# Kernel tuning notes

Hardware: AMD Instinct MI355X
Metric: run time of the kernel (lower is better)

The kernel has to match this reference:

```python
import jax, jax.numpy as jnp
import numpy as np

D = 1024

def setup_inputs() -> dict:
    key = jax.random.key(0)
    ks = jax.random.split(key, 7)
    x = jax.random.normal(ks[0], (8, 2048, D), dtype=jnp.float32)
    s = 1.0 / np.sqrt(D)
    Wq = jax.random.normal(ks[1], (D, D), dtype=jnp.float32) * s
    Wk = jax.random.normal(ks[2], (D, D), dtype=jnp.float32) * s
    Wv = jax.random.normal(ks[3], (D, D), dtype=jnp.float32) * s
    bq = jax.random.normal(ks[4], (D,), dtype=jnp.float32) * 0.01
    bk = jax.random.normal(ks[5], (D,), dtype=jnp.float32) * 0.01
    bv = jax.random.normal(ks[6], (D,), dtype=jnp.float32) * 0.01
    return {"x": x, "Wq": Wq, "bq": bq, "Wk": Wk, "bk": bk, "Wv": Wv, "bv": bv}

def reference(x, Wq, bq, Wk, bk, Wv, bv):
    # x: [b, s, d]; Linear stored as [d_in, d_out]
    Q = jnp.einsum('bsd,de->bse', x, Wq) + bq
    K = jnp.einsum('bsd,de->bse', x, Wk) + bk
    V = jnp.einsum('bsd,de->bse', x, Wv) + bv
    scale = 1.0 / jnp.sqrt(jnp.float32(x.shape[-1]))
    scores = jnp.einsum('bqd,bkd->bqk', Q, K) * scale  # [b, s, s]
    attn = jax.nn.softmax(scores, axis=-1)
    return jnp.einsum('bqk,bkd->bqd', attn, V)
```

## Files before the change

kernel.cpp:

```cpp
#include <hip/hip_runtime.h>
#include <hip/hip_bf16.h>
#include <stdint.h>

typedef __bf16 bf16x8 __attribute__((ext_vector_type(8)));
typedef float  f32x4  __attribute__((ext_vector_type(4)));

#define AS1 __attribute__((address_space(1)))
#define AS3 __attribute__((address_space(3)))

__device__ __forceinline__ void gemm_mainloop_256(
    const __hip_bfloat16* __restrict__ A,
    const __hip_bfloat16* __restrict__ B,
    int K, int m0, int n0, f32x4 acc[8][4])
{
    __shared__ __hip_bfloat16 As[2][256 * 64];
    __shared__ __hip_bfloat16 Bs[2][256 * 64];

    const int tid  = threadIdx.x;
    const int lane = tid & 63;
    const int w    = tid >> 6;
    const int wr   = w >> 2;
    const int wc   = w & 3;
    const int fr   = lane & 15;
    const int fq   = lane >> 4;
    const int lr   = lane >> 3;
    const int swz  = ((lane & 7) ^ lr) * 8;

    #pragma unroll
    for (int rt = 0; rt < 8; ++rt)
        #pragma unroll
        for (int ct = 0; ct < 4; ++ct)
            acc[rt][ct] = (f32x4){0.f, 0.f, 0.f, 0.f};

    const __hip_bfloat16* gA = A + (long)(m0 + w * 8 + lr) * K + swz;
    const __hip_bfloat16* gB = B + (long)(n0 + w * 8 + lr) * K + swz;
    const int ldsBase = (w * 8) * 64;
    const int NT = K >> 6;

#define STAGE(T, BUF)                                                        \
    {                                                                        \
        const long koff = (long)(T) * 64;                                    \
        _Pragma("unroll")                                                    \
        for (int i = 0; i < 4; ++i) {                                        \
            __builtin_amdgcn_global_load_lds(                                \
                (AS1 void*)(void*)(gA + (long)i * 64 * K + koff),            \
                (AS3 void*)(&As[BUF][ldsBase + i * 64 * 64]), 16, 0, 0);     \
            __builtin_amdgcn_global_load_lds(                                \
                (AS1 void*)(void*)(gB + (long)i * 64 * K + koff),            \
                (AS3 void*)(&Bs[BUF][ldsBase + i * 64 * 64]), 16, 0, 0);     \
        }                                                                    \
    }

    STAGE(0, 0);
    STAGE(1, 1);
    asm volatile("s_waitcnt vmcnt(8)" ::: "memory");
    __builtin_amdgcn_sched_barrier(0);
    __builtin_amdgcn_s_barrier();
    __builtin_amdgcn_sched_barrier(0);

    int cur = 0;
    for (int t = 0; t < NT; ++t) {
        #pragma unroll
        for (int ks = 0; ks < 2; ++ks) {
            const int colOff = ((ks * 4 + fq) ^ (fr & 7)) * 8;
            bf16x8 af[8], bfv[4];
            #pragma unroll
            for (int rt = 0; rt < 8; ++rt)
                af[rt] = *(const bf16x8*)&As[cur][(wr * 128 + rt * 16 + fr) * 64 + colOff];
            #pragma unroll
            for (int ct = 0; ct < 4; ++ct)
                bfv[ct] = *(const bf16x8*)&Bs[cur][(wc * 64 + ct * 16 + fr) * 64 + colOff];
            __builtin_amdgcn_s_setprio(1);
            #pragma unroll
            for (int rt = 0; rt < 8; ++rt)
                #pragma unroll
                for (int ct = 0; ct < 4; ++ct)
                    acc[rt][ct] = __builtin_amdgcn_mfma_f32_16x16x32_bf16(
                        af[rt], bfv[ct], acc[rt][ct], 0, 0, 0);
            __builtin_amdgcn_s_setprio(0);
        }
        if (t == NT - 1) break;
        __builtin_amdgcn_s_barrier();
        __builtin_amdgcn_sched_barrier(0);
        if (t + 2 < NT) {
            STAGE(t + 2, cur);
            asm volatile("s_waitcnt vmcnt(8)" ::: "memory");
        } else {
            asm volatile("s_waitcnt vmcnt(0)" ::: "memory");
        }
        __builtin_amdgcn_sched_barrier(0);
        __builtin_amdgcn_s_barrier();
        __builtin_amdgcn_sched_barrier(0);
        cur ^= 1;
    }
#undef STAGE
}

__global__ __launch_bounds__(256) void k_castx(const float* __restrict__ x,
                                               __hip_bfloat16* __restrict__ xb)
{
    int i = blockIdx.x * 256 + threadIdx.x;
    float4 f = ((const float4*)x)[i];
    union { uint2 u; __hip_bfloat16 h[4]; } o;
    o.h[0] = __float2bfloat16(f.x);
    o.h[1] = __float2bfloat16(f.y);
    o.h[2] = __float2bfloat16(f.z);
    o.h[3] = __float2bfloat16(f.w);
    ((uint2*)xb)[i] = o.u;
}

__global__ __launch_bounds__(256) void k_wt(const float* __restrict__ Wq,
                                            const float* __restrict__ Wk,
                                            const float* __restrict__ Wv,
                                            __hip_bfloat16* __restrict__ Wt)
{
    __shared__ float t[32][33];
    const float* W = (blockIdx.z == 0) ? Wq : (blockIdx.z == 1 ? Wk : Wv);
    const int d0 = blockIdx.y * 32, e0 = blockIdx.x * 32;
    #pragma unroll
    for (int j = 0; j < 4; ++j)
        t[threadIdx.y + j * 8][threadIdx.x] =
            W[(long)(d0 + threadIdx.y + j * 8) * 1024 + e0 + threadIdx.x];
    __syncthreads();
    __hip_bfloat16* dst = Wt + (long)blockIdx.z * 1024 * 1024;
    #pragma unroll
    for (int j = 0; j < 4; ++j)
        dst[(long)(e0 + threadIdx.y + j * 8) * 1024 + d0 + threadIdx.x] =
            __float2bfloat16(t[threadIdx.x][threadIdx.y + j * 8]);
}

__global__ __launch_bounds__(256) void k_zero(float* __restrict__ p)
{
    p[blockIdx.x * 256 + threadIdx.x] = 0.f;
}

__global__ __launch_bounds__(512, 2) void k_qkv(
    const __hip_bfloat16* __restrict__ xb, const __hip_bfloat16* __restrict__ Wt,
    __hip_bfloat16* __restrict__ Qb, __hip_bfloat16* __restrict__ Kb,
    __hip_bfloat16* __restrict__ Vt,
    const float* __restrict__ bq, const float* __restrict__ bk,
    const float* __restrict__ bv)
{
    f32x4 acc[8][4];
    const int n0 = blockIdx.x * 256;
    const int m0 = blockIdx.y * 256;
    gemm_mainloop_256(xb, Wt, 1024, m0, n0, acc);

    const int lane = threadIdx.x & 63, w = threadIdx.x >> 6;
    const int wr = w >> 2, wc = w & 3, fr = lane & 15, fq = lane >> 4;
    const int mat  = n0 >> 10;
    const int rowB = m0 + wr * 128;

    if (mat < 2) {
        __hip_bfloat16* out = (mat == 0) ? Qb : Kb;
        const float* bias   = (mat == 0) ? bq : bk;
        #pragma unroll
        for (int ct = 0; ct < 4; ++ct) {
            const int e = (n0 & 1023) + wc * 64 + ct * 16 + fr;
            const float bval = bias[e];
            #pragma unroll
            for (int rt = 0; rt < 8; ++rt) {
                const int r0 = rowB + rt * 16 + fq * 4;
                #pragma unroll
                for (int r = 0; r < 4; ++r)
                    out[(long)(r0 + r) * 1024 + e] =
                        __float2bfloat16(acc[rt][ct][r] + bval);
            }
        }
    } else {
        #pragma unroll
        for (int ct = 0; ct < 4; ++ct) {
            const int e = (n0 & 1023) + wc * 64 + ct * 16 + fr;
            const float bval = bv[e];
            #pragma unroll
            for (int rt = 0; rt < 8; ++rt) {
                const int r0 = rowB + rt * 16 + fq * 4;
                const int bz = r0 >> 11, s0 = r0 & 2047;
                union { ushort4 v; __hip_bfloat16 h[4]; } pk;
                #pragma unroll
                for (int r = 0; r < 4; ++r)
                    pk.h[r] = __float2bfloat16(acc[rt][ct][r] + bval);
                *(ushort4*)&Vt[(long)bz * 2097152 + (long)e * 2048 + s0] = pk.v;
            }
        }
    }
}

__global__ __launch_bounds__(512, 2) void k_scores(
    const __hip_bfloat16* __restrict__ Qb, const __hip_bfloat16* __restrict__ Kb,
    __hip_bfloat16* __restrict__ Sb, float* __restrict__ rs)
{
    f32x4 acc[8][4];
    const int z  = blockIdx.z;
    const int n0 = blockIdx.x * 256;
    const int m0 = blockIdx.y * 256;
    gemm_mainloop_256(Qb + (long)z * 2048 * 1024,
                      Kb + (long)z * 2048 * 1024, 1024, m0, n0, acc);

    __hip_bfloat16* out = Sb + (long)z * 2048 * 2048;
    float* rsz = rs + z * 2048;
    const int lane = threadIdx.x & 63, w = threadIdx.x >> 6;
    const int wr = w >> 2, wc = w & 3, fr = lane & 15, fq = lane >> 4;

    #pragma unroll
    for (int rt = 0; rt < 8; ++rt) {
        const int r0 = m0 + wr * 128 + rt * 16 + fq * 4;
        float psum[4] = {0.f, 0.f, 0.f, 0.f};
        #pragma unroll
        for (int ct = 0; ct < 4; ++ct) {
            const int col = n0 + wc * 64 + ct * 16 + fr;
            #pragma unroll
            for (int r = 0; r < 4; ++r) {
                const float p = __expf(acc[rt][ct][r] * 0.03125f);
                psum[r] += p;
                out[(long)(r0 + r) * 2048 + col] = __float2bfloat16(p);
            }
        }
        #pragma unroll
        for (int r = 0; r < 4; ++r) {
            float v = psum[r];
            v += __shfl_xor(v, 1, 16);
            v += __shfl_xor(v, 2, 16);
            v += __shfl_xor(v, 4, 16);
            v += __shfl_xor(v, 8, 16);
            if (fr == 0) atomicAdd(&rsz[r0 + r], v);
        }
    }
}

__global__ __launch_bounds__(512, 2) void k_pv(
    const __hip_bfloat16* __restrict__ Pb, const __hip_bfloat16* __restrict__ Vt,
    const float* __restrict__ rs, float* __restrict__ O)
{
    f32x4 acc[8][4];
    const int z  = blockIdx.z;
    const int n0 = blockIdx.x * 256;
    const int m0 = blockIdx.y * 256;
    gemm_mainloop_256(Pb + (long)z * 2048 * 2048,
                      Vt + (long)z * 1024 * 2048, 2048, m0, n0, acc);

    float* out = O + (long)z * 2048 * 1024;
    const float* rsz = rs + z * 2048;
    const int lane = threadIdx.x & 63, w = threadIdx.x >> 6;
    const int wr = w >> 2, wc = w & 3, fr = lane & 15, fq = lane >> 4;

    #pragma unroll
    for (int rt = 0; rt < 8; ++rt) {
        const int r0 = m0 + wr * 128 + rt * 16 + fq * 4;
        const float4 rv = *(const float4*)&rsz[r0];
        f32x4 inv;
        inv[0] = 1.f / rv.x; inv[1] = 1.f / rv.y;
        inv[2] = 1.f / rv.z; inv[3] = 1.f / rv.w;
        #pragma unroll
        for (int ct = 0; ct < 4; ++ct) {
            const int col = n0 + wc * 64 + ct * 16 + fr;
            #pragma unroll
            for (int r = 0; r < 4; ++r)
                out[(long)(r0 + r) * 1024 + col] = acc[rt][ct][r] * inv[r];
        }
    }
}

extern "C" void kernel_launch(void* const* d_in, const int* in_sizes, int n_in,
                              void* d_out, int out_size, void* d_ws, size_t ws_size,
                              hipStream_t stream)
{
    const float* x  = (const float*)d_in[0];
    const float* Wq = (const float*)d_in[1];
    const float* bq = (const float*)d_in[2];
    const float* Wk = (const float*)d_in[3];
    const float* bk = (const float*)d_in[4];
    const float* Wv = (const float*)d_in[5];
    const float* bv = (const float*)d_in[6];
    float* out = (float*)d_out;

    uint8_t* ws = (uint8_t*)d_ws;
    __hip_bfloat16* xb = (__hip_bfloat16*)(ws + 0);
    __hip_bfloat16* Wt = (__hip_bfloat16*)(ws + 33554432);
    __hip_bfloat16* Qb = (__hip_bfloat16*)(ws + 39845888);
    __hip_bfloat16* Kb = (__hip_bfloat16*)(ws + 73400320);
    __hip_bfloat16* Vt = (__hip_bfloat16*)(ws + 106954752);
    __hip_bfloat16* Sb = (__hip_bfloat16*)(ws + 140509184);
    float* rs = (float*)(ws + 33554432);

    k_castx<<<16384, 256, 0, stream>>>(x, xb);
    k_wt<<<dim3(32, 32, 3), dim3(32, 8), 0, stream>>>(Wq, Wk, Wv, Wt);
    k_qkv<<<dim3(12, 64), 512, 0, stream>>>(xb, Wt, Qb, Kb, Vt, bq, bk, bv);
    k_zero<<<64, 256, 0, stream>>>(rs);
    k_scores<<<dim3(8, 8, 8), 512, 0, stream>>>(Qb, Kb, Sb, rs);
    k_pv<<<dim3(4, 8, 8), 512, 0, stream>>>(Sb, Vt, rs, out);
}
```

Measured before the change: 404.4 us.

## Shrink GEMM tiles to 128x128 single-buffered with XCD-aware block swizzle

Replaces the 256x256 double-buffered GEMM mainloop with a 128x128 tile, 4-wave, single-buffered loop that uses plain __syncthreads, and raises occupancy targets to 3 blocks per CU. Adds an XCD block-index swizzle so that neighbouring tiles land on the same chiplet for L2 reuse. Grids grow fourfold. The change drops the async prefetch overlap and the setprio scheduling hints, and smaller tiles lower arithmetic intensity per LDS load.

```diff
diff --git a/kernel.cpp b/kernel.cpp
--- a/kernel.cpp
+++ b/kernel.cpp
@@ -8,92 +8,71 @@
 #define AS1 __attribute__((address_space(1)))
 #define AS3 __attribute__((address_space(3)))
 
-__device__ __forceinline__ void gemm_mainloop_256(
+__device__ __forceinline__ void gemm_mainloop_128(
     const __hip_bfloat16* __restrict__ A,
     const __hip_bfloat16* __restrict__ B,
-    int K, int m0, int n0, f32x4 acc[8][4])
-{
-    __shared__ __hip_bfloat16 As[2][256 * 64];
-    __shared__ __hip_bfloat16 Bs[2][256 * 64];
+    int K, int m0, int n0, f32x4 acc[4][4])
+{
+    __shared__ __hip_bfloat16 As[128 * 64];
+    __shared__ __hip_bfloat16 Bs[128 * 64];
 
     const int tid  = threadIdx.x;
     const int lane = tid & 63;
     const int w    = tid >> 6;
-    const int wr   = w >> 2;
-    const int wc   = w & 3;
+    const int wm   = (w >> 1) * 64;
+    const int wn   = (w & 1) * 64;
     const int fr   = lane & 15;
     const int fq   = lane >> 4;
-    const int lr   = lane >> 3;
-    const int swz  = ((lane & 7) ^ lr) * 8;
-
-    #pragma unroll
-    for (int rt = 0; rt < 8; ++rt)
+    const int ldRow = lane >> 3;
+    const int ldCol = ((lane & 7) ^ ldRow) * 8;
+
+    #pragma unroll
+    for (int rt = 0; rt < 4; ++rt)
         #pragma unroll
         for (int ct = 0; ct < 4; ++ct)
             acc[rt][ct] = (f32x4){0.f, 0.f, 0.f, 0.f};
 
-    const __hip_bfloat16* gA = A + (long)(m0 + w * 8 + lr) * K + swz;
-    const __hip_bfloat16* gB = B + (long)(n0 + w * 8 + lr) * K + swz;
-    const int ldsBase = (w * 8) * 64;
-    const int NT = K >> 6;
-
-#define STAGE(T, BUF)                                                        \
-    {                                                                        \
-        const long koff = (long)(T) * 64;                                    \
-        _Pragma("unroll")                                                    \
-        for (int i = 0; i < 4; ++i) {                                        \
-            __builtin_amdgcn_global_load_lds(                                \
-                (AS1 void*)(void*)(gA + (long)i * 64 * K + koff),            \
-                (AS3 void*)(&As[BUF][ldsBase + i * 64 * 64]), 16, 0, 0);     \
-            __builtin_amdgcn_global_load_lds(                                \
-                (AS1 void*)(void*)(gB + (long)i * 64 * K + koff),            \
-                (AS3 void*)(&Bs[BUF][ldsBase + i * 64 * 64]), 16, 0, 0);     \
-        }                                                                    \
-    }
-
-    STAGE(0, 0);
-    STAGE(1, 1);
-    asm volatile("s_waitcnt vmcnt(8)" ::: "memory");
-    __builtin_amdgcn_sched_barrier(0);
-    __builtin_amdgcn_s_barrier();
-    __builtin_amdgcn_sched_barrier(0);
-
-    int cur = 0;
-    for (int t = 0; t < NT; ++t) {
+    for (int k0 = 0; k0 < K; k0 += 64) {
+        #pragma unroll
+        for (int c = 0; c < 4; ++c) {
+            const int rbase = w * 32 + c * 8;
+            const __hip_bfloat16* gA = A + (long)(m0 + rbase + ldRow) * K + (k0 + ldCol);
+            const __hip_bfloat16* gB = B + (long)(n0 + rbase + ldRow) * K + (k0 + ldCol);
+            __builtin_amdgcn_global_load_lds((AS1 void*)(void*)gA,
+                                             (AS3 void*)(&As[rbase * 64]), 16, 0, 0);
+            __builtin_amdgcn_global_load_lds((AS1 void*)(void*)gB,
+                                             (AS3 void*)(&Bs[rbase * 64]), 16, 0, 0);
+        }
+        __syncthreads();
+
         #pragma unroll
         for (int ks = 0; ks < 2; ++ks) {
             const int colOff = ((ks * 4 + fq) ^ (fr & 7)) * 8;
-            bf16x8 af[8], bfv[4];
-            #pragma unroll
-            for (int rt = 0; rt < 8; ++rt)
-                af[rt] = *(const bf16x8*)&As[cur][(wr * 128 + rt * 16 + fr) * 64 + colOff];
-            #pragma unroll
-            for (int ct = 0; ct < 4; ++ct)
-                bfv[ct] = *(const bf16x8*)&Bs[cur][(wc * 64 + ct * 16 + fr) * 64 + colOff];
-            __builtin_amdgcn_s_setprio(1);
-            #pragma unroll
-            for (int rt = 0; rt < 8; ++rt)
+            bf16x8 af[4], bfr[4];
+            #pragma unroll
+            for (int t = 0; t < 4; ++t) {
+                af[t]  = *(const bf16x8*)&As[(wm + t * 16 + fr) * 64 + colOff];
+                bfr[t] = *(const bf16x8*)&Bs[(wn + t * 16 + fr) * 64 + colOff];
+            }
+            #pragma unroll
+            for (int rt = 0; rt < 4; ++rt)
                 #pragma unroll
                 for (int ct = 0; ct < 4; ++ct)
                     acc[rt][ct] = __builtin_amdgcn_mfma_f32_16x16x32_bf16(
-                        af[rt], bfv[ct], acc[rt][ct], 0, 0, 0);
-            __builtin_amdgcn_s_setprio(0);
-        }
-        if (t == NT - 1) break;
-        __builtin_amdgcn_s_barrier();
-        __builtin_amdgcn_sched_barrier(0);
-        if (t + 2 < NT) {
-            STAGE(t + 2, cur);
-            asm volatile("s_waitcnt vmcnt(8)" ::: "memory");
-        } else {
-            asm volatile("s_waitcnt vmcnt(0)" ::: "memory");
-        }
-        __builtin_amdgcn_sched_barrier(0);
-        __builtin_amdgcn_s_barrier();
-        __builtin_amdgcn_sched_barrier(0);
-        cur ^= 1;
-    }
-#undef STAGE
+                        af[rt], bfr[ct], acc[rt][ct], 0, 0, 0);
+        }
+        __syncthreads();
+    }
+}
+
+__device__ __forceinline__ void xcd_swizzle(int gx, int gy, int& bx, int& by)
+{
+    const int n   = gx * gy;
+    const int lin = by * gx + bx;
+    const int q   = n >> 3;
+    const int s   = (lin & 7) * q + (lin >> 3);
+    bx = s % gx;
+    by = s / gx;
 }
 
 __global__ __launch_bounds__(256) void k_castx(const float* __restrict__ x,
@@ -134,33 +113,35 @@
     p[blockIdx.x * 256 + threadIdx.x] = 0.f;
 }
 
-__global__ __launch_bounds__(512, 2) void k_qkv(
+__global__ __launch_bounds__(256, 3) void k_qkv(
     const __hip_bfloat16* __restrict__ xb, const __hip_bfloat16* __restrict__ Wt,
     __hip_bfloat16* __restrict__ Qb, __hip_bfloat16* __restrict__ Kb,
     __hip_bfloat16* __restrict__ Vt,
     const float* __restrict__ bq, const float* __restrict__ bk,
     const float* __restrict__ bv)
 {
-    f32x4 acc[8][4];
-    const int n0 = blockIdx.x * 256;
-    const int m0 = blockIdx.y * 256;
-    gemm_mainloop_256(xb, Wt, 1024, m0, n0, acc);
+    f32x4 acc[4][4];
+    int bx = blockIdx.x, by = blockIdx.y;
+    xcd_swizzle(gridDim.x, gridDim.y, bx, by);
+    const int n0 = bx * 128;
+    const int m0 = by * 128;
+    gemm_mainloop_128(xb, Wt, 1024, m0, n0, acc);
 
     const int lane = threadIdx.x & 63, w = threadIdx.x >> 6;
-    const int wr = w >> 2, wc = w & 3, fr = lane & 15, fq = lane >> 4;
-    const int mat  = n0 >> 10;
-    const int rowB = m0 + wr * 128;
+    const int wm = (w >> 1) * 64, wn = (w & 1) * 64;
+    const int fr = lane & 15, fq = lane >> 4;
+    const int mat = n0 >> 10;
 
     if (mat < 2) {
         __hip_bfloat16* out = (mat == 0) ? Qb : Kb;
         const float* bias   = (mat == 0) ? bq : bk;
         #pragma unroll
         for (int ct = 0; ct < 4; ++ct) {
-            const int e = (n0 & 1023) + wc * 64 + ct * 16 + fr;
+            const int e = (n0 & 1023) + wn + ct * 16 + fr;
             const float bval = bias[e];
             #pragma unroll
-            for (int rt = 0; rt < 8; ++rt) {
-                const int r0 = rowB + rt * 16 + fq * 4;
+            for (int rt = 0; rt < 4; ++rt) {
+                const int r0 = m0 + wm + rt * 16 + fq * 4;
                 #pragma unroll
                 for (int r = 0; r < 4; ++r)
                     out[(long)(r0 + r) * 1024 + e] =
@@ -170,11 +151,11 @@
     } else {
         #pragma unroll
         for (int ct = 0; ct < 4; ++ct) {
-            const int e = (n0 & 1023) + wc * 64 + ct * 16 + fr;
+            const int e = (n0 & 1023) + wn + ct * 16 + fr;
             const float bval = bv[e];
             #pragma unroll
-            for (int rt = 0; rt < 8; ++rt) {
-                const int r0 = rowB + rt * 16 + fq * 4;
+            for (int rt = 0; rt < 4; ++rt) {
+                const int r0 = m0 + wm + rt * 16 + fq * 4;
                 const int bz = r0 >> 11, s0 = r0 & 2047;
                 union { ushort4 v; __hip_bfloat16 h[4]; } pk;
                 #pragma unroll
@@ -186,29 +167,32 @@
     }
 }
 
-__global__ __launch_bounds__(512, 2) void k_scores(
+__global__ __launch_bounds__(256, 3) void k_scores(
     const __hip_bfloat16* __restrict__ Qb, const __hip_bfloat16* __restrict__ Kb,
     __hip_bfloat16* __restrict__ Sb, float* __restrict__ rs)
 {
-    f32x4 acc[8][4];
+    f32x4 acc[4][4];
     const int z  = blockIdx.z;
-    const int n0 = blockIdx.x * 256;
-    const int m0 = blockIdx.y * 256;
-    gemm_mainloop_256(Qb + (long)z * 2048 * 1024,
+    int bx = blockIdx.x, by = blockIdx.y;
+    xcd_swizzle(gridDim.x, gridDim.y, bx, by);
+    const int n0 = bx * 128;
+    const int m0 = by * 128;
+    gemm_mainloop_128(Qb + (long)z * 2048 * 1024,
                       Kb + (long)z * 2048 * 1024, 1024, m0, n0, acc);
 
     __hip_bfloat16* out = Sb + (long)z * 2048 * 2048;
     float* rsz = rs + z * 2048;
     const int lane = threadIdx.x & 63, w = threadIdx.x >> 6;
-    const int wr = w >> 2, wc = w & 3, fr = lane & 15, fq = lane >> 4;
-
-    #pragma unroll
-    for (int rt = 0; rt < 8; ++rt) {
-        const int r0 = m0 + wr * 128 + rt * 16 + fq * 4;
+    const int wm = (w >> 1) * 64, wn = (w & 1) * 64;
+    const int fr = lane & 15, fq = lane >> 4;
+
+    #pragma unroll
+    for (int rt = 0; rt < 4; ++rt) {
+        const int r0 = m0 + wm + rt * 16 + fq * 4;
         float psum[4] = {0.f, 0.f, 0.f, 0.f};
         #pragma unroll
         for (int ct = 0; ct < 4; ++ct) {
-            const int col = n0 + wc * 64 + ct * 16 + fr;
+            const int col = n0 + wn + ct * 16 + fr;
             #pragma unroll
             for (int r = 0; r < 4; ++r) {
                 const float p = __expf(acc[rt][ct][r] * 0.03125f);
@@ -228,32 +212,35 @@
     }
 }
 
-__global__ __launch_bounds__(512, 2) void k_pv(
+__global__ __launch_bounds__(256, 3) void k_pv(
     const __hip_bfloat16* __restrict__ Pb, const __hip_bfloat16* __restrict__ Vt,
     const float* __restrict__ rs, float* __restrict__ O)
 {
-    f32x4 acc[8][4];
+    f32x4 acc[4][4];
     const int z  = blockIdx.z;
-    const int n0 = blockIdx.x * 256;
-    const int m0 = blockIdx.y * 256;
-    gemm_mainloop_256(Pb + (long)z * 2048 * 2048,
+    int bx = blockIdx.x, by = blockIdx.y;
+    xcd_swizzle(gridDim.x, gridDim.y, bx, by);
+    const int n0 = bx * 128;
+    const int m0 = by * 128;
+    gemm_mainloop_128(Pb + (long)z * 2048 * 2048,
                       Vt + (long)z * 1024 * 2048, 2048, m0, n0, acc);
 
     float* out = O + (long)z * 2048 * 1024;
     const float* rsz = rs + z * 2048;
     const int lane = threadIdx.x & 63, w = threadIdx.x >> 6;
-    const int wr = w >> 2, wc = w & 3, fr = lane & 15, fq = lane >> 4;
-
-    #pragma unroll
-    for (int rt = 0; rt < 8; ++rt) {
-        const int r0 = m0 + wr * 128 + rt * 16 + fq * 4;
+    const int wm = (w >> 1) * 64, wn = (w & 1) * 64;
+    const int fr = lane & 15, fq = lane >> 4;
+
+    #pragma unroll
+    for (int rt = 0; rt < 4; ++rt) {
+        const int r0 = m0 + wm + rt * 16 + fq * 4;
         const float4 rv = *(const float4*)&rsz[r0];
         f32x4 inv;
         inv[0] = 1.f / rv.x; inv[1] = 1.f / rv.y;
         inv[2] = 1.f / rv.z; inv[3] = 1.f / rv.w;
         #pragma unroll
         for (int ct = 0; ct < 4; ++ct) {
-            const int col = n0 + wc * 64 + ct * 16 + fr;
+            const int col = n0 + wn + ct * 16 + fr;
             #pragma unroll
             for (int r = 0; r < 4; ++r)
                 out[(long)(r0 + r) * 1024 + col] = acc[rt][ct][r] * inv[r];
@@ -285,8 +272,8 @@
 
     k_castx<<<16384, 256, 0, stream>>>(x, xb);
     k_wt<<<dim3(32, 32, 3), dim3(32, 8), 0, stream>>>(Wq, Wk, Wv, Wt);
-    k_qkv<<<dim3(12, 64), 512, 0, stream>>>(xb, Wt, Qb, Kb, Vt, bq, bk, bv);
+    k_qkv<<<dim3(24, 128), 256, 0, stream>>>(xb, Wt, Qb, Kb, Vt, bq, bk, bv);
     k_zero<<<64, 256, 0, stream>>>(rs);
-    k_scores<<<dim3(8, 8, 8), 512, 0, stream>>>(Qb, Kb, Sb, rs);
-    k_pv<<<dim3(4, 8, 8), 512, 0, stream>>>(Sb, Vt, rs, out);
-}
+    k_scores<<<dim3(16, 16, 8), 256, 0, stream>>>(Qb, Kb, Sb, rs);
+    k_pv<<<dim3(8, 16, 8), 256, 0, stream>>>(Sb, Vt, rs, out);
+}
```

Result: no change. 397.3 us (-1.8%).
